# Performance work log

Hardware: AMD Instinct MI355X
Metric: run time of the kernel (lower is better)

## Reference

```python
import jax, jax.numpy as jnp
import numpy as np

B, S, D, H = 4, 1024, 1024, 16
HS = D // H  # head_size = 64


def setup_inputs() -> dict:
    key = jax.random.key(0)
    ks = jax.random.split(key, 12)
    sc_d = 1.0 / np.sqrt(D)
    sc_h = 1.0 / np.sqrt(HS)
    inp = {
        "queries": jax.random.normal(ks[0], (B, S, D), jnp.float32),
        "keys": jax.random.normal(ks[1], (B, S, D), jnp.float32),
        "values": jax.random.normal(ks[2], (B, S, D), jnp.float32),
        # causal mask: scores where mask == 0 are filled with -1e9
        "mask": jnp.tril(jnp.ones((S, S), jnp.int32)),
        # per-head query/key projections: [H, D, HS] weights, [H, HS] biases
        "Wq": jax.random.uniform(ks[3], (H, D, HS), jnp.float32, -sc_d, sc_d),
        "bq": jax.random.uniform(ks[4], (H, HS), jnp.float32, -sc_d, sc_d),
        "Wk": jax.random.uniform(ks[5], (H, D, HS), jnp.float32, -sc_d, sc_d),
        "bk": jax.random.uniform(ks[6], (H, HS), jnp.float32, -sc_d, sc_d),
        # shared value projection: [D, HS]
        "Wv": jax.random.uniform(ks[7], (D, HS), jnp.float32, -sc_d, sc_d),
        "bv": jax.random.uniform(ks[8], (HS,), jnp.float32, -sc_d, sc_d),
        # output projection: [HS, D]
        "Wo": jax.random.uniform(ks[9], (HS, D), jnp.float32, -sc_h, sc_h),
        "bo": jax.random.uniform(ks[10], (D,), jnp.float32, -sc_h, sc_h),
    }
    return inp


def reference(queries, keys, values, mask, Wq, bq, Wk, bk, Wv, bv, Wo, bo):
    # shared value projection: [B, S, HS]
    v = jnp.einsum("bsd,de->bse", values, Wv) + bv
    # batched per-head projections (replaces the python loop over heads)
    q = jnp.einsum("bsd,hde->bhse", queries, Wq) + bq[None, :, None, :]
    k = jnp.einsum("btd,hde->bhte", keys, Wk) + bk[None, :, None, :]
    scores = jnp.einsum("bhse,bhte->bhst", q, k) / jnp.sqrt(jnp.float32(HS))
    scores = jnp.where(mask == 0, jnp.float32(-1e9), scores)
    attn = jax.nn.softmax(scores, axis=-1)  # [B, H, S, S]; dropout = eval-mode identity
    head_out = jnp.einsum("bhst,bte->bhse", attn, v)
    out = head_out.mean(axis=1)  # mean over heads -> [B, S, HS]
    out = jnp.einsum("bse,ed->bsd", out, Wo) + bo
    attention_weights = attn.mean(axis=1)  # [B, S, S]
    return out, attention_weights
```

## Files before the change

kernel.cpp:

```cpp
#include <hip/hip_runtime.h>
#include <hip/hip_bf16.h>
#include <stdint.h>

typedef _Float16 half8 __attribute__((ext_vector_type(8)));
typedef _Float16 half4 __attribute__((ext_vector_type(4)));
typedef float    f32x4 __attribute__((ext_vector_type(4)));

#define MFMA16(a, b, c) __builtin_amdgcn_mfma_f32_16x16x32_f16(a, b, c, 0, 0, 0)

typedef __attribute__((address_space(1))) const void GVOID;
typedef __attribute__((address_space(3))) void LVOID;
__device__ __forceinline__ void glds16(const void* g, void* l)
{
    __builtin_amdgcn_global_load_lds((GVOID*)g, (LVOID*)l, 16, 0, 0);
}

#define BARRIER() do { asm volatile("" ::: "memory"); \
    __builtin_amdgcn_s_barrier(); \
    asm volatile("" ::: "memory"); } while (0)

__global__ __launch_bounds__(256) void transpose_to_f16(
    const float* __restrict__ X, _Float16* __restrict__ Y,
    int R, int C, long inBS, long outBS)
{
    __shared__ float t[32][33];
    const int bz = blockIdx.z;
    X += (long)bz * inBS;
    Y += (long)bz * outBS;
    const int c0 = blockIdx.x * 32, r0 = blockIdx.y * 32;
    const int tx = threadIdx.x & 31, ty = threadIdx.x >> 5;
#pragma unroll
    for (int i = 0; i < 4; ++i)
        t[ty + i * 8][tx] = X[(long)(r0 + ty + i * 8) * C + c0 + tx];
    __syncthreads();
#pragma unroll
    for (int i = 0; i < 4; ++i)
        Y[(long)(c0 + ty + i * 8) * R + r0 + tx] = (_Float16)t[tx][ty + i * 8];
}

__global__ __launch_bounds__(256) void cvt_qk_f16(
    const float* __restrict__ S0, const float* __restrict__ S1,
    _Float16* __restrict__ D)
{
    const float* S = blockIdx.y ? S1 : S0;
    _Float16* Dz = D + (long)blockIdx.y * 4194304;
    const long i = ((long)blockIdx.x * 256 + threadIdx.x) * 8;
    const float4 v0 = *(const float4*)(S + i);
    const float4 v1 = *(const float4*)(S + i + 4);
    half8 h;
    h[0] = (_Float16)v0.x; h[1] = (_Float16)v0.y;
    h[2] = (_Float16)v0.z; h[3] = (_Float16)v0.w;
    h[4] = (_Float16)v1.x; h[5] = (_Float16)v1.y;
    h[6] = (_Float16)v1.z; h[7] = (_Float16)v1.w;
    *(half8*)(Dz + i) = h;
}

__global__ __launch_bounds__(256, 2) void gemm_qk_glds(
    const _Float16* __restrict__ A16,
    const _Float16* __restrict__ BT,
    const float* __restrict__ bias0, const float* __restrict__ bias1,
    _Float16* __restrict__ Cout)
{
    __shared__ __align__(16) _Float16 As[2][128 * 64];
    __shared__ __align__(16) _Float16 Bs[2][128 * 64];

    const int gx  = gridDim.x, gy = gridDim.y;
    const int nwg = gx * gy * (int)gridDim.z;
    const int lid = (int)blockIdx.x + gx * ((int)blockIdx.y + gy * (int)blockIdx.z);
    const int q8  = nwg >> 3;
    const int xcd = lid & 7, loc = lid >> 3;
    const int sw  = xcd * q8 + loc;
    const int nt  = sw % gx;
    const int tm2 = sw / gx;
    const int mt  = tm2 % gy;
    const int z   = tm2 / gy;

    const int n0 = nt * 128;
    const int m0 = mt * 128;
    const int tid  = threadIdx.x;
    const int wave = tid >> 6, lane = tid & 63;
    const int m16  = lane & 15, quad = lane >> 4;

    const char* Az = (const char*)(A16 + (long)z * 4194304);
    const char* Bz = (const char*)(BT  + (long)z * 1048576);

    const int colbyte = (((lane & 7) ^ (lane >> 3)) << 4);
    const char* gaBase = Az + ((long)(m0 + wave * 32 + (lane >> 3)) << 11) + colbyte;
    const char* gbBase = Bz + ((long)(n0 + wave * 32 + (lane >> 3)) << 11) + colbyte;

    f32x4 acc[2][8];
    {
        f32x4 zz = {0.f, 0.f, 0.f, 0.f};
#pragma unroll
        for (int i = 0; i < 2; ++i)
#pragma unroll
            for (int j = 0; j < 8; ++j) acc[i][j] = zz;
    }

    auto STAGE = [&](int bf, int k0) {
        const char* ga = gaBase + (k0 << 1);
        const char* gb = gbBase + (k0 << 1);
        _Float16* la = &As[bf][wave * 32 * 64];
        _Float16* lb = &Bs[bf][wave * 32 * 64];
#pragma unroll
        for (int i = 0; i < 4; ++i) {
            glds16(ga + (long)i * 8 * 2048, la + i * 8 * 64);
            glds16(gb + (long)i * 8 * 2048, lb + i * 8 * 64);
        }
    };

    auto COMPUTE = [&](int bf) {
        const char* Ab = (const char*)&As[bf][0];
        const char* Bp = (const char*)&Bs[bf][0];
        const int sw4 = (m16 & 7) << 4;
#pragma unroll
        for (int kss = 0; kss < 2; ++kss) {
            const int kbs = (kss * 64 + quad * 16) ^ sw4;
            const half8 a0 = *(const half8*)(Ab + (wave * 32 + m16) * 128 + kbs);
            const half8 a1 = *(const half8*)(Ab + (wave * 32 + 16 + m16) * 128 + kbs);
#pragma unroll
            for (int c = 0; c < 8; ++c) {
                const half8 bfr = *(const half8*)(Bp + (c * 16 + m16) * 128 + kbs);
                acc[0][c] = MFMA16(a0, bfr, acc[0][c]);
                acc[1][c] = MFMA16(a1, bfr, acc[1][c]);
            }
        }
    };

    STAGE(0, 0);
    STAGE(1, 64);
    int cur = 0;
    for (int t = 0; t < 15; ++t) {
        asm volatile("s_waitcnt vmcnt(8)" ::: "memory");
        __builtin_amdgcn_sched_barrier(0);
        BARRIER();
        COMPUTE(cur);
        BARRIER();
        if (t < 14) STAGE(cur, (t + 2) * 64);
        cur ^= 1;
    }
    asm volatile("s_waitcnt vmcnt(0)" ::: "memory");
    __builtin_amdgcn_sched_barrier(0);
    BARRIER();
    COMPUTE(cur);

    const float* bias = z ? bias1 : bias0;
    _Float16* Cz = Cout + (long)z * 4194304;
#pragma unroll
    for (int hh = 0; hh < 2; ++hh) {
#pragma unroll
        for (int c = 0; c < 8; ++c) {
            const int col = n0 + c * 16 + m16;
            const float bb = bias[col];
#pragma unroll
            for (int r = 0; r < 4; ++r) {
                const int row = m0 + wave * 32 + hh * 16 + quad * 4 + r;
                Cz[(long)row * 1024 + col] = (_Float16)(acc[hh][c][r] + bb);
            }
        }
    }
}

__global__ __launch_bounds__(256, 2) void gemm_f16_v2(
    const float* __restrict__ A0, const float* __restrict__ A1,
    const _Float16* __restrict__ BT,
    const float* __restrict__ bias0, const float* __restrict__ bias1,
    void* __restrict__ Cout,
    int N, int lda, int ldbt, int ldc,
    long aBS, long bBS, long cBS,
    int c_half, int atomic, int nks, int kchunk)
{
    __shared__ __align__(16) _Float16 As[128][72];
    __shared__ __align__(16) _Float16 Bs[128][72];

    const int gx  = gridDim.x, gy = gridDim.y;
    const int nwg = gx * gy * (int)gridDim.z;
    const int lid = (int)blockIdx.x + gx * ((int)blockIdx.y + gy * (int)blockIdx.z);
    const int q8  = nwg >> 3, r8 = nwg & 7;
    const int xcd = lid & 7, loc = lid >> 3;
    const int sw  = (xcd < r8 ? xcd * (q8 + 1) : r8 * (q8 + 1) + (xcd - r8) * q8) + loc;
    const int nt  = sw % gx;
    const int tm2 = sw / gx;
    const int mt  = tm2 % gy;
    const int bz  = tm2 / gy;

    const int b = bz / nks, ks = bz % nks;
    const int kbeg = ks * kchunk;
    const int kend = kbeg + kchunk;

    const float* A = A1 ? (b ? A1 : A0) : (A0 + (long)b * aBS);
    const _Float16* Bb = BT + (long)b * bBS;

    const int n0 = nt * 128;
    const int m0 = mt * 128;
    const int tid  = threadIdx.x;
    const int wave = tid >> 6, lane = tid & 63;
    const int m16  = lane & 15, quad = lane >> 4;

    const int acol = (tid & 15) * 4;
    const int arb  = tid >> 4;
    const int bj   = tid >> 1;
    const int bcc  = (tid & 1) * 32;
    int jn = n0 + bj; if (jn > N - 1) jn = N - 1;
    const _Float16* bpB = Bb + (long)jn * ldbt;

    f32x4 acc[2][8];
    {
        f32x4 zz = {0.f, 0.f, 0.f, 0.f};
#pragma unroll
        for (int i = 0; i < 2; ++i)
#pragma unroll
            for (int j = 0; j < 8; ++j) acc[i][j] = zz;
    }

    for (int k0 = kbeg; k0 < kend; k0 += 64) {
        {
            float4 av[8];
#pragma unroll
            for (int p = 0; p < 8; ++p)
                av[p] = *(const float4*)(A + (long)(m0 + arb + p * 16) * lda + k0 + acol);
#pragma unroll
            for (int p = 0; p < 8; ++p) {
                half4 hv;
                hv[0] = (_Float16)av[p].x; hv[1] = (_Float16)av[p].y;
                hv[2] = (_Float16)av[p].z; hv[3] = (_Float16)av[p].w;
                *(half4*)&As[arb + p * 16][acol] = hv;
            }
        }
        {
            const _Float16* bp = bpB + k0 + bcc;
            half8 b0 = *(const half8*)(bp);
            half8 b1 = *(const half8*)(bp + 8);
            half8 b2 = *(const half8*)(bp + 16);
            half8 b3 = *(const half8*)(bp + 24);
            *(half8*)&Bs[bj][bcc]      = b0;
            *(half8*)&Bs[bj][bcc + 8]  = b1;
            *(half8*)&Bs[bj][bcc + 16] = b2;
            *(half8*)&Bs[bj][bcc + 24] = b3;
        }
        __syncthreads();
#pragma unroll
        for (int kss = 0; kss < 2; ++kss) {
            const int ko = kss * 32 + quad * 8;
            const half8 a0 = *(const half8*)&As[wave * 32 + m16][ko];
            const half8 a1 = *(const half8*)&As[wave * 32 + 16 + m16][ko];
#pragma unroll
            for (int c = 0; c < 8; ++c) {
                const half8 bf = *(const half8*)&Bs[c * 16 + m16][ko];
                acc[0][c] = MFMA16(a0, bf, acc[0][c]);
                acc[1][c] = MFMA16(a1, bf, acc[1][c]);
            }
        }
        __syncthreads();
    }

    const float* bias = b ? bias1 : bias0;
    const int addb = (bias != nullptr) && (kbeg == 0);
#pragma unroll
    for (int hh = 0; hh < 2; ++hh) {
#pragma unroll
        for (int c = 0; c < 8; ++c) {
            const int col = n0 + c * 16 + m16;
            if (col >= N) continue;
            const float bb = addb ? bias[col] : 0.f;
#pragma unroll
            for (int r = 0; r < 4; ++r) {
                const int row = m0 + wave * 32 + hh * 16 + quad * 4 + r;
                const float v = acc[hh][c][r] + bb;
                const long idx = (long)b * cBS + (long)row * ldc + col;
                if (atomic)      atomicAdd(&((float*)Cout)[idx], v);
                else if (c_half) ((_Float16*)Cout)[idx] = (_Float16)v;
                else             ((float*)Cout)[idx] = v;
            }
        }
    }
}

__global__ __launch_bounds__(256, 4) void attn_stats(
    const _Float16* __restrict__ q_all, const _Float16* __restrict__ k_all,
    float* __restrict__ m_out, float* __restrict__ il_out)
{
    const int st = blockIdx.x, h = blockIdx.y, b = blockIdx.z;
    const int tid = threadIdx.x, wave = tid >> 6, lane = tid & 63;
    const int m16 = lane & 15, quad = lane >> 4;
    const int s0 = st * 64;
    const int sw = s0 + wave * 16;

    __shared__ __align__(16) _Float16 qs[64][72];
    __shared__ __align__(16) _Float16 ks[64][72];

    const int srow = tid >> 2;
    const int scol = (tid & 3) * 16;

    {
        const _Float16* qsrc = q_all + ((long)(b * 1024 + s0 + srow)) * 1024 + h * 64 + scol;
        *(half8*)&qs[srow][scol]     = *(const half8*)(qsrc);
        *(half8*)&qs[srow][scol + 8] = *(const half8*)(qsrc + 8);
    }

    const _Float16* ksrcb = k_all + ((long)(b * 1024 + srow)) * 1024 + h * 64 + scol;

    float mr[4], lr[4];
#pragma unroll
    for (int r = 0; r < 4; ++r) { mr[r] = -3.0e38f; lr[r] = 0.f; }

    half8 a0, a1;
    for (int tt = 0; tt <= st; ++tt) {
        const _Float16* ksrc = ksrcb + (long)(tt * 64) * 1024;
        const half8 k0 = *(const half8*)(ksrc);
        const half8 k1 = *(const half8*)(ksrc + 8);

        __syncthreads();
        *(half8*)&ks[srow][scol]     = k0;
        *(half8*)&ks[srow][scol + 8] = k1;
        __syncthreads();

        if (tt == 0) {
            a0 = *(const half8*)&qs[wave * 16 + m16][quad * 8];
            a1 = *(const half8*)&qs[wave * 16 + m16][quad * 8 + 32];
        }

        if (tt < st) {
#pragma unroll
            for (int c = 0; c < 4; ++c) {
                const half8 b0 = *(const half8*)&ks[c * 16 + m16][quad * 8];
                const half8 b1 = *(const half8*)&ks[c * 16 + m16][quad * 8 + 32];
                f32x4 cc = {0.f, 0.f, 0.f, 0.f};
                cc = MFMA16(a0, b0, cc);
                cc = MFMA16(a1, b1, cc);
#pragma unroll
                for (int r = 0; r < 4; ++r) {
                    const float zz = cc[r] * 0.125f;
                    const float nm = fmaxf(mr[r], zz);
                    lr[r] = lr[r] * __expf(mr[r] - nm) + __expf(zz - nm);
                    mr[r] = nm;
                }
            }
        } else {
#pragma unroll
            for (int c = 0; c < 4; ++c) {
                const half8 b0 = *(const half8*)&ks[c * 16 + m16][quad * 8];
                const half8 b1 = *(const half8*)&ks[c * 16 + m16][quad * 8 + 32];
                f32x4 cc = {0.f, 0.f, 0.f, 0.f};
                cc = MFMA16(a0, b0, cc);
                cc = MFMA16(a1, b1, cc);
                const int col = tt * 64 + c * 16 + m16;
#pragma unroll
                for (int r = 0; r < 4; ++r) {
                    const int row = sw + quad * 4 + r;
                    if (col <= row) {
                        const float zz = cc[r] * 0.125f;
                        const float nm = fmaxf(mr[r], zz);
                        lr[r] = lr[r] * __expf(mr[r] - nm) + __expf(zz - nm);
                        mr[r] = nm;
                    }
                }
            }
        }
    }

#pragma unroll
    for (int mk = 1; mk < 16; mk <<= 1) {
#pragma unroll
        for (int r = 0; r < 4; ++r) {
            const float om = __shfl_xor(mr[r], mk);
            const float ol = __shfl_xor(lr[r], mk);
            const float nm = fmaxf(mr[r], om);
            lr[r] = lr[r] * __expf(mr[r] - nm) + ol * __expf(om - nm);
            mr[r] = nm;
        }
    }
    if (m16 == 0) {
#pragma unroll
        for (int r = 0; r < 4; ++r) {
            const long idx = ((long)(b * 16 + h)) * 1024 + sw + quad * 4 + r;
            m_out[idx]  = mr[r];
            il_out[idx] = 1.f / lr[r];
        }
    }
}

__global__ __launch_bounds__(256, 3) void attn_pmean(
    const _Float16* __restrict__ q_all, const _Float16* __restrict__ k_all,
    const float* __restrict__ m_in, const float* __restrict__ il_in,
    const _Float16* __restrict__ vT,
    float* __restrict__ attn,
    float* __restrict__ ctx)
{
    const int ttile = blockIdx.x, stile = blockIdx.y, b = blockIdx.z;
    const int tid = threadIdx.x;
    if (ttile > stile) {
        const int c4 = (tid & 15) * 4;
        float4 zz = {0.f, 0.f, 0.f, 0.f};
#pragma unroll
        for (int i = 0; i < 4; ++i) {
            const int r = stile * 64 + (tid >> 4) + i * 16;
            *(float4*)&attn[((long)(b * 1024 + r)) * 1024 + ttile * 64 + c4] = zz;
        }
        return;
    }

    __shared__ __align__(16) _Float16 qs2[2][64 * 64];
    __shared__ __align__(16) _Float16 ks2[2][64 * 64];
    __shared__ __align__(16) _Float16 ps[64][72];
    __shared__ __align__(16) float mls[16][64];
    __shared__ __align__(16) float ils[16][64];

    const int wave = tid >> 6, lane = tid & 63;
    const int m16 = lane & 15, quad = lane >> 4;
    const int s0 = stile * 64;
    const int t0 = ttile * 64;
    const int sw = s0 + wave * 16;
    const int diag = (ttile == stile);

    {
        const int hh = tid >> 4;
        const int c4 = (tid & 15) * 4;
        const long ix = ((long)(b * 16 + hh)) * 1024 + s0 + c4;
        const float4 mv4 = *(const float4*)&m_in[ix];
        const float4 iv4 = *(const float4*)&il_in[ix];
        *(float4*)&mls[hh][c4] = mv4;
        *(float4*)&ils[hh][c4] = iv4;
    }

    const int colb = (((lane & 7) ^ (lane >> 3)) << 4);
    const char* gq = (const char*)q_all + ((long)(b * 1024 + s0 + wave * 16 + (lane >> 3)) << 11) + colb;
    const char* gk = (const char*)k_all + ((long)(b * 1024 + t0 + wave * 16 + (lane >> 3)) << 11) + colb;

    auto STAGE_P = [&](int bf, int h) {
        const char* q = gq + h * 128;
        const char* k = gk + h * 128;
        _Float16* lq = &qs2[bf][wave * 16 * 64];
        _Float16* lk = &ks2[bf][wave * 16 * 64];
        glds16(q, lq);
        glds16(q + 8 * 2048, lq + 8 * 64);
        glds16(k, lk);
        glds16(k + 8 * 2048, lk + 8 * 64);
    };

    STAGE_P(0, 0);
    STAGE_P(1, 1);
    asm volatile("s_waitcnt lgkmcnt(0)" ::: "memory");
    BARRIER();

    float pm[4][4];
#pragma unroll
    for (int c = 0; c < 4; ++c)
#pragma unroll
        for (int r = 0; r < 4; ++r) pm[c][r] = 0.f;

    const int swz = (m16 & 7) << 4;
    int cur = 0;

    auto COMPUTE_H = [&](int h, int bf) {
        const char* Qc = (const char*)&qs2[bf][0];
        const char* Kc = (const char*)&ks2[bf][0];
        const half8 a0 = *(const half8*)(Qc + (wave * 16 + m16) * 128 + ((quad * 16) ^ swz));
        const half8 a1 = *(const half8*)(Qc + (wave * 16 + m16) * 128 + ((quad * 16 + 64) ^ swz));
        const float4 mv = *(const float4*)&mls[h][wave * 16 + quad * 4];
        const float4 iv = *(const float4*)&ils[h][wave * 16 + quad * 4];
        const float mrow[4] = {mv.x, mv.y, mv.z, mv.w};
        const float irow[4] = {iv.x, iv.y, iv.z, iv.w};
        if (!diag) {
#pragma unroll
            for (int c = 0; c < 4; ++c) {
                const half8 b0 = *(const half8*)(Kc + (c * 16 + m16) * 128 + ((quad * 16) ^ swz));
                const half8 b1 = *(const half8*)(Kc + (c * 16 + m16) * 128 + ((quad * 16 + 64) ^ swz));
                f32x4 cc = {0.f, 0.f, 0.f, 0.f};
                cc = MFMA16(a0, b0, cc);
                cc = MFMA16(a1, b1, cc);
#pragma unroll
                for (int r = 0; r < 4; ++r)
                    pm[c][r] += __expf(cc[r] * 0.125f - mrow[r]) * irow[r];
            }
        } else {
#pragma unroll
            for (int c = 0; c < 4; ++c) {
                const half8 b0 = *(const half8*)(Kc + (c * 16 + m16) * 128 + ((quad * 16) ^ swz));
                const half8 b1 = *(const half8*)(Kc + (c * 16 + m16) * 128 + ((quad * 16 + 64) ^ swz));
                f32x4 cc = {0.f, 0.f, 0.f, 0.f};
                cc = MFMA16(a0, b0, cc);
                cc = MFMA16(a1, b1, cc);
                const int col = t0 + c * 16 + m16;
#pragma unroll
                for (int r = 0; r < 4; ++r) {
                    const int row = sw + quad * 4 + r;
                    if (col <= row)
                        pm[c][r] += __expf(cc[r] * 0.125f - mrow[r]) * irow[r];
                }
            }
        }
    };

    for (int h = 0; h < 15; ++h) {
        asm volatile("s_waitcnt vmcnt(4)" ::: "memory");
        __builtin_amdgcn_sched_barrier(0);
        BARRIER();
        COMPUTE_H(h, cur);
        BARRIER();
        if (h < 14) STAGE_P(cur, h + 2);
        cur ^= 1;
    }
    asm volatile("s_waitcnt vmcnt(0)" ::: "memory");
    __builtin_amdgcn_sched_barrier(0);
    BARRIER();
    COMPUTE_H(15, cur);

#pragma unroll
    for (int c = 0; c < 4; ++c) {
#pragma unroll
        for (int r = 0; r < 4; ++r) {
            const int rloc = (wave << 4) + (quad << 2) + r;
            const int cloc = c * 16 + m16;
            const float p = pm[c][r] * 0.0625f;
            attn[((long)(b * 1024 + s0 + rloc)) * 1024 + t0 + cloc] = p;
            ps[rloc][cloc] = (_Float16)p;
        }
    }
    __syncthreads();

    const _Float16* vTb = vT + (long)b * 65536 + t0;
    f32x4 apv[4];
    {
        f32x4 zz = {0.f, 0.f, 0.f, 0.f};
#pragma unroll
        for (int c = 0; c < 4; ++c) apv[c] = zz;
    }
#pragma unroll
    for (int kss = 0; kss < 2; ++kss) {
        const half8 a = *(const half8*)&ps[wave * 16 + m16][kss * 32 + quad * 8];
#pragma unroll
        for (int c = 0; c < 4; ++c) {
            const half8 bf = *(const half8*)(vTb + (long)(c * 16 + m16) * 1024 + kss * 32 + quad * 8);
            apv[c] = MFMA16(a, bf, apv[c]);
        }
    }
#pragma unroll
    for (int c = 0; c < 4; ++c) {
#pragma unroll
        for (int r = 0; r < 4; ++r) {
            const int row = sw + quad * 4 + r;
            const int e   = c * 16 + m16;
            atomicAdd(&ctx[((long)(b * 1024 + row)) * 64 + e], apv[c][r]);
        }
    }
}

extern "C" void kernel_launch(void* const* d_in, const int* in_sizes, int n_in,
                              void* d_out, int out_size, void* d_ws, size_t ws_size,
                              hipStream_t stream)
{
    const float* queries = (const float*)d_in[0];
    const float* keys    = (const float*)d_in[1];
    const float* values  = (const float*)d_in[2];
    const float* Wq = (const float*)d_in[4];
    const float* bq = (const float*)d_in[5];
    const float* Wk = (const float*)d_in[6];
    const float* bk = (const float*)d_in[7];
    const float* Wv = (const float*)d_in[8];
    const float* bv = (const float*)d_in[9];
    const float* Wo = (const float*)d_in[10];
    const float* bo = (const float*)d_in[11];

    float* out_ptr  = (float*)d_out;
    float* attn_ptr = out_ptr + (long)4096 * 1024;

    uint8_t* w = (uint8_t*)d_ws;
    size_t off = 0;
    auto alloc = [&](size_t bytes) {
        void* p = w + off;
        off = (off + bytes + 255) & ~(size_t)255;
        return p;
    };
    _Float16* WqkT  = (_Float16*)alloc((size_t)2 * 1024 * 1024 * 2);
    _Float16* WvT   = (_Float16*)alloc((size_t)64 * 1024 * 2);
    _Float16* WoT   = (_Float16*)alloc((size_t)1024 * 64 * 2);
    _Float16* qkall = (_Float16*)alloc((size_t)2 * 4194304 * 2);
    _Float16* a16   = (_Float16*)alloc((size_t)2 * 4194304 * 2);
    float*    vbuf  = (float*)alloc((size_t)4096 * 64 * 4);
    _Float16* vT    = (_Float16*)alloc((size_t)4 * 64 * 1024 * 2);
    float*    ctx   = (float*)alloc((size_t)4096 * 64 * 4);
    float*    mbuf  = (float*)alloc((size_t)65536 * 4);
    float*    ilbuf = (float*)alloc((size_t)65536 * 4);
    (void)ws_size; (void)in_sizes; (void)n_in; (void)out_size;

    _Float16* qall = qkall;
    _Float16* kall = qkall + (long)4194304;

    transpose_to_f16<<<dim3(2, 32, 16), 256, 0, stream>>>(Wq, WqkT, 1024, 64, 65536, 65536);
    transpose_to_f16<<<dim3(2, 32, 16), 256, 0, stream>>>(Wk, WqkT + (long)1024 * 1024, 1024, 64, 65536, 65536);
    transpose_to_f16<<<dim3(2, 32, 1),  256, 0, stream>>>(Wv, WvT, 1024, 64, 0, 0);
    transpose_to_f16<<<dim3(32, 2, 1),  256, 0, stream>>>(Wo, WoT, 64, 1024, 0, 0);
    cvt_qk_f16<<<dim3(2048, 2, 1), 256, 0, stream>>>(queries, keys, a16);

    gemm_qk_glds<<<dim3(8, 32, 2), 256, 0, stream>>>(
        a16, WqkT, bq, bk, qkall);

    hipMemsetAsync(vbuf, 0, (size_t)4096 * 64 * 4, stream);
    gemm_f16_v2<<<dim3(1, 32, 8), 256, 0, stream>>>(
        values, nullptr, WvT, bv, nullptr, vbuf,
        64, 1024, 1024, 64,
        0, 0, 0,
        0, 1, 8, 128);

    transpose_to_f16<<<dim3(2, 32, 4), 256, 0, stream>>>(vbuf, vT, 1024, 64, 65536, 65536);

    hipMemsetAsync(ctx, 0, (size_t)4096 * 64 * 4, stream);
    attn_stats<<<dim3(16, 16, 4), 256, 0, stream>>>(qall, kall, mbuf, ilbuf);
    attn_pmean<<<dim3(16, 16, 4), 256, 0, stream>>>(qall, kall, mbuf, ilbuf, vT, attn_ptr, ctx);

    gemm_f16_v2<<<dim3(8, 32, 1), 256, 0, stream>>>(
        ctx, nullptr, WoT, bo, nullptr, out_ptr,
        1024, 64, 64, 1024,
        0, 0, 0,
        0, 0, 1, 64);
}
```

Measured before the change: 241.5 us.

## Fuse prep launches and memsets into one kernel; process two key tiles per stats step

Merges the four weight transposes, the query/key f16 conversion, the two memsets and the zeroing of the whole attention output into a single prep_all launch, which cuts launch overhead. The upper-triangle zero stores in attn_pmean are dropped, because that kernel now only returns early for those tiles. attn_stats now loads two 64-row key tiles per barrier pair, halving the number of synchronisations. The trade-off is that prep_all writes the full 16MB attn buffer, including regions attn_pmean overwrites later, and the stats inner loop is no longer fully unrolled.

```diff
diff --git a/kernel.cpp b/kernel.cpp
--- a/kernel.cpp
+++ b/kernel.cpp
@@ -18,6 +18,74 @@
 #define BARRIER() do { asm volatile("" ::: "memory"); \
     __builtin_amdgcn_s_barrier(); \
     asm volatile("" ::: "memory"); } while (0)
+
+__global__ __launch_bounds__(256) void prep_all(
+    const float* __restrict__ Wq, const float* __restrict__ Wk,
+    const float* __restrict__ Wv, const float* __restrict__ Wo,
+    const float* __restrict__ queries, const float* __restrict__ keys,
+    _Float16* __restrict__ WqkT, _Float16* __restrict__ WvT,
+    _Float16* __restrict__ WoT, _Float16* __restrict__ a16,
+    float* __restrict__ vbuf, float* __restrict__ ctx,
+    float* __restrict__ attn)
+{
+    __shared__ float t[32][33];
+    const int id = blockIdx.x;
+    const int tid = threadIdx.x;
+
+    if (id < 2176) {
+        const float* X; _Float16* Y; int R, C, bx, by;
+        if (id < 2048) {
+            const int isK = id >> 10;
+            const int local = id & 1023;
+            bx = local & 1;
+            by = (local >> 1) & 31;
+            const int hz = local >> 6;
+            X = (isK ? Wk : Wq) + (long)hz * 65536;
+            Y = WqkT + (long)isK * 1048576 + (long)hz * 65536;
+            R = 1024; C = 64;
+        } else if (id < 2112) {
+            const int local = id - 2048;
+            bx = local & 1; by = local >> 1;
+            X = Wv; Y = WvT; R = 1024; C = 64;
+        } else {
+            const int local = id - 2112;
+            bx = local & 31; by = local >> 5;
+            X = Wo; Y = WoT; R = 64; C = 1024;
+        }
+        const int c0 = bx * 32, r0 = by * 32;
+        const int tx = tid & 31, ty = tid >> 5;
+#pragma unroll
+        for (int i = 0; i < 4; ++i)
+            t[ty + i * 8][tx] = X[(long)(r0 + ty + i * 8) * C + c0 + tx];
+        __syncthreads();
+#pragma unroll
+        for (int i = 0; i < 4; ++i)
+            Y[(long)(c0 + ty + i * 8) * R + r0 + tx] = (_Float16)t[tx][ty + i * 8];
+    } else if (id < 6272) {
+        const int isK = (id - 2176) >> 11;
+        const int local = (id - 2176) & 2047;
+        const float* S = isK ? keys : queries;
+        _Float16* Dz = a16 + (long)isK * 4194304;
+        const long i = ((long)local * 256 + tid) * 8;
+        const float4 v0 = *(const float4*)(S + i);
+        const float4 v1 = *(const float4*)(S + i + 4);
+        half8 h;
+        h[0] = (_Float16)v0.x; h[1] = (_Float16)v0.y;
+        h[2] = (_Float16)v0.z; h[3] = (_Float16)v0.w;
+        h[4] = (_Float16)v1.x; h[5] = (_Float16)v1.y;
+        h[6] = (_Float16)v1.z; h[7] = (_Float16)v1.w;
+        *(half8*)(Dz + i) = h;
+    } else if (id < 6528) {
+        const float4 z = {0.f, 0.f, 0.f, 0.f};
+        ((float4*)vbuf)[(long)(id - 6272) * 256 + tid] = z;
+    } else if (id < 6784) {
+        const float4 z = {0.f, 0.f, 0.f, 0.f};
+        ((float4*)ctx)[(long)(id - 6528) * 256 + tid] = z;
+    } else {
+        const float4 z = {0.f, 0.f, 0.f, 0.f};
+        ((float4*)attn)[(long)(id - 6784) * 256 + tid] = z;
+    }
+}
 
 __global__ __launch_bounds__(256) void transpose_to_f16(
     const float* __restrict__ X, _Float16* __restrict__ Y,
@@ -36,23 +104,6 @@
 #pragma unroll
     for (int i = 0; i < 4; ++i)
         Y[(long)(c0 + ty + i * 8) * R + r0 + tx] = (_Float16)t[tx][ty + i * 8];
-}
-
-__global__ __launch_bounds__(256) void cvt_qk_f16(
-    const float* __restrict__ S0, const float* __restrict__ S1,
-    _Float16* __restrict__ D)
-{
-    const float* S = blockIdx.y ? S1 : S0;
-    _Float16* Dz = D + (long)blockIdx.y * 4194304;
-    const long i = ((long)blockIdx.x * 256 + threadIdx.x) * 8;
-    const float4 v0 = *(const float4*)(S + i);
-    const float4 v1 = *(const float4*)(S + i + 4);
-    half8 h;
-    h[0] = (_Float16)v0.x; h[1] = (_Float16)v0.y;
-    h[2] = (_Float16)v0.z; h[3] = (_Float16)v0.w;
-    h[4] = (_Float16)v1.x; h[5] = (_Float16)v1.y;
-    h[6] = (_Float16)v1.z; h[7] = (_Float16)v1.w;
-    *(half8*)(Dz + i) = h;
 }
 
 __global__ __launch_bounds__(256, 2) void gemm_qk_glds(
@@ -287,7 +338,7 @@
     const int sw = s0 + wave * 16;
 
     __shared__ __align__(16) _Float16 qs[64][72];
-    __shared__ __align__(16) _Float16 ks[64][72];
+    __shared__ __align__(16) _Float16 ks[128][72];
 
     const int srow = tid >> 2;
     const int scol = (tid & 3) * 16;
@@ -305,29 +356,43 @@
     for (int r = 0; r < 4; ++r) { mr[r] = -3.0e38f; lr[r] = 0.f; }
 
     half8 a0, a1;
-    for (int tt = 0; tt <= st; ++tt) {
-        const _Float16* ksrc = ksrcb + (long)(tt * 64) * 1024;
-        const half8 k0 = *(const half8*)(ksrc);
-        const half8 k1 = *(const half8*)(ksrc + 8);
+    for (int ch = 0; 2 * ch <= st; ++ch) {
+        const int tbase = 2 * ch;
+        const int two = (tbase + 1 <= st);
+
+        const _Float16* ksrc0 = ksrcb + (long)(tbase * 64) * 1024;
+        const half8 k0 = *(const half8*)(ksrc0);
+        const half8 k1 = *(const half8*)(ksrc0 + 8);
+        half8 k2, k3;
+        if (two) {
+            const _Float16* ksrc1 = ksrc0 + (long)64 * 1024;
+            k2 = *(const half8*)(ksrc1);
+            k3 = *(const half8*)(ksrc1 + 8);
+        }
 
         __syncthreads();
         *(half8*)&ks[srow][scol]     = k0;
         *(half8*)&ks[srow][scol + 8] = k1;
+        if (two) {
+            *(half8*)&ks[64 + srow][scol]     = k2;
+            *(half8*)&ks[64 + srow][scol + 8] = k3;
+        }
         __syncthreads();
 
-        if (tt == 0) {
+        if (ch == 0) {
             a0 = *(const half8*)&qs[wave * 16 + m16][quad * 8];
             a1 = *(const half8*)&qs[wave * 16 + m16][quad * 8 + 32];
         }
 
-        if (tt < st) {
-#pragma unroll
-            for (int c = 0; c < 4; ++c) {
-                const half8 b0 = *(const half8*)&ks[c * 16 + m16][quad * 8];
-                const half8 b1 = *(const half8*)&ks[c * 16 + m16][quad * 8 + 32];
-                f32x4 cc = {0.f, 0.f, 0.f, 0.f};
-                cc = MFMA16(a0, b0, cc);
-                cc = MFMA16(a1, b1, cc);
+        const int ncol = two ? 8 : 4;
+        for (int c = 0; c < ncol; ++c) {
+            const half8 b0 = *(const half8*)&ks[c * 16 + m16][quad * 8];
+            const half8 b1 = *(const half8*)&ks[c * 16 + m16][quad * 8 + 32];
+            f32x4 cc = {0.f, 0.f, 0.f, 0.f};
+            cc = MFMA16(a0, b0, cc);
+            cc = MFMA16(a1, b1, cc);
+            const int tile = tbase + (c >> 2);
+            if (tile < st) {
 #pragma unroll
                 for (int r = 0; r < 4; ++r) {
                     const float zz = cc[r] * 0.125f;
@@ -335,16 +400,8 @@
                     lr[r] = lr[r] * __expf(mr[r] - nm) + __expf(zz - nm);
                     mr[r] = nm;
                 }
-            }
-        } else {
-#pragma unroll
-            for (int c = 0; c < 4; ++c) {
-                const half8 b0 = *(const half8*)&ks[c * 16 + m16][quad * 8];
-                const half8 b1 = *(const half8*)&ks[c * 16 + m16][quad * 8 + 32];
-                f32x4 cc = {0.f, 0.f, 0.f, 0.f};
-                cc = MFMA16(a0, b0, cc);
-                cc = MFMA16(a1, b1, cc);
-                const int col = tt * 64 + c * 16 + m16;
+            } else {
+                const int col = tile * 64 + (c & 3) * 16 + m16;
 #pragma unroll
                 for (int r = 0; r < 4; ++r) {
                     const int row = sw + quad * 4 + r;
@@ -389,16 +446,7 @@
 {
     const int ttile = blockIdx.x, stile = blockIdx.y, b = blockIdx.z;
     const int tid = threadIdx.x;
-    if (ttile > stile) {
-        const int c4 = (tid & 15) * 4;
-        float4 zz = {0.f, 0.f, 0.f, 0.f};
-#pragma unroll
-        for (int i = 0; i < 4; ++i) {
-            const int r = stile * 64 + (tid >> 4) + i * 16;
-            *(float4*)&attn[((long)(b * 1024 + r)) * 1024 + ttile * 64 + c4] = zz;
-        }
-        return;
-    }
+    if (ttile > stile) return;
 
     __shared__ __align__(16) _Float16 qs2[2][64 * 64];
     __shared__ __align__(16) _Float16 ks2[2][64 * 64];
@@ -587,16 +635,13 @@
     _Float16* qall = qkall;
     _Float16* kall = qkall + (long)4194304;
 
-    transpose_to_f16<<<dim3(2, 32, 16), 256, 0, stream>>>(Wq, WqkT, 1024, 64, 65536, 65536);
-    transpose_to_f16<<<dim3(2, 32, 16), 256, 0, stream>>>(Wk, WqkT + (long)1024 * 1024, 1024, 64, 65536, 65536);
-    transpose_to_f16<<<dim3(2, 32, 1),  256, 0, stream>>>(Wv, WvT, 1024, 64, 0, 0);
-    transpose_to_f16<<<dim3(32, 2, 1),  256, 0, stream>>>(Wo, WoT, 64, 1024, 0, 0);
-    cvt_qk_f16<<<dim3(2048, 2, 1), 256, 0, stream>>>(queries, keys, a16);
+    prep_all<<<dim3(10880, 1, 1), 256, 0, stream>>>(
+        Wq, Wk, Wv, Wo, queries, keys,
+        WqkT, WvT, WoT, a16, vbuf, ctx, attn_ptr);
 
     gemm_qk_glds<<<dim3(8, 32, 2), 256, 0, stream>>>(
         a16, WqkT, bq, bk, qkall);
 
-    hipMemsetAsync(vbuf, 0, (size_t)4096 * 64 * 4, stream);
     gemm_f16_v2<<<dim3(1, 32, 8), 256, 0, stream>>>(
         values, nullptr, WvT, bv, nullptr, vbuf,
         64, 1024, 1024, 64,
@@ -605,7 +650,6 @@
 
     transpose_to_f16<<<dim3(2, 32, 4), 256, 0, stream>>>(vbuf, vT, 1024, 64, 65536, 65536);
 
-    hipMemsetAsync(ctx, 0, (size_t)4096 * 64 * 4, stream);
     attn_stats<<<dim3(16, 16, 4), 256, 0, stream>>>(qall, kall, mbuf, ilbuf);
     attn_pmean<<<dim3(16, 16, 4), 256, 0, stream>>>(qall, kall, mbuf, ilbuf, vT, attn_ptr, ctx);
 
```

Result: faster. 235.5 us (-2.5%).
